# Performance work log

Measured on AMD Instinct MI355X. Metric: run time of the kernel, lower is better.

The kernel has to match this reference:

```python
import jax, jax.numpy as jnp
import numpy as np

B, L, FD = 16, 196, 2048      # batch, fmap locations (14x14), resnet101 feat dim
N, WD, HD, DD = 1000, 300, 512, 5  # n_class, word_dim, hid_dim, d_dim
E, TMAX, NIMG = 50000, 5, 1000     # n_edges, gru steps, imagenet classes


def setup_inputs():
    key = jax.random.key(0)
    ks = jax.random.split(key, 32)
    p = lambda k, s: (jax.random.normal(k, s, jnp.float32) * 0.02)
    z = lambda n: jnp.zeros((n,), jnp.float32)
    return {
        'feats': jax.random.normal(ks[0], (B, L, FD), jnp.float32),
        'embed': jax.random.normal(ks[1], (N, WD), jnp.float32),
        'edges': jax.random.randint(ks[2], (2, E), 0, N, jnp.int32),
        # attention key/query nets
        'W_key': p(ks[3], (FD, HD)), 'b_key': z(HD),
        'W_query': p(ks[4], (WD, HD)), 'b_query': z(HD),
        # F_in: feat_dim -> 512 -> d_dim (relu)
        'Wf1': p(ks[5], (FD, 512)), 'bf1': z(512),
        'Wf2': p(ks[6], (512, DD)), 'bf2': z(DD),
        # F_rel: 2*word_dim -> 256 -> 1 (relu)
        'Wr1': p(ks[7], (2 * WD, 256)), 'br1': z(256),
        'Wr2': p(ks[8], (256, 1)), 'br2': z(1),
        # F_out: d_dim -> 512 -> 1 (relu)
        'Wo1': p(ks[9], (DD, 512)), 'bo1': z(512),
        'Wo2': p(ks[10], (512, 1)), 'bo2': z(1),
        # GRUCell (torch layout: [3*d, d] stacked r,z,n)
        'W_ih': p(ks[11], (3 * DD, DD)), 'b_ih': z(3 * DD),
        'W_hh': p(ks[12], (3 * DD, DD)), 'b_hh': z(3 * DD),
        # imagenet classifier on pooled features
        'W_clf': p(ks[13], (FD, NIMG)), 'b_clf': z(NIMG),
    }


def _gru_cell(x, h, W_ih, W_hh, b_ih, b_hh):
    gi = x @ W_ih.T + b_ih            # [M, 3d]
    gh = h @ W_hh.T + b_hh
    i_r, i_z, i_n = jnp.split(gi, 3, axis=-1)
    h_r, h_z, h_n = jnp.split(gh, 3, axis=-1)
    r = jax.nn.sigmoid(i_r + h_r)
    zg = jax.nn.sigmoid(i_z + h_z)
    n = jnp.tanh(i_n + r * h_n)
    return (1.0 - zg) * n + zg * h


def reference(feats, embed, edges, W_key, b_key, W_query, b_query,
              Wf1, bf1, Wf2, bf2, Wr1, br1, Wr2, br2, Wo1, bo1, Wo2, bo2,
              W_ih, b_ih, W_hh, b_hh, W_clf, b_clf):
    # imagenet scores from globally pooled backbone features
    pooled = jnp.mean(feats, axis=1)                      # [B, FD]
    imgnet_scores = jax.nn.softmax(pooled @ W_clf + b_clf, axis=1)

    # label-conditional spatial attention
    keys = feats @ W_key + b_key                          # [B, L, HD]
    queries = embed @ W_query + b_query                   # [N, HD]
    scores = jnp.einsum('blh,nh->bnl', keys, queries)     # [B, N, L]
    attn = jax.nn.softmax(scores, axis=2)
    graph_input = jnp.einsum('bnl,blf->bnf', attn, feats) # [B, N, FD]
    graph_input = graph_input.reshape(-1, FD)             # [B*N, FD]

    # F_in MLP -> initial hidden state
    h0 = jax.nn.relu(graph_input @ Wf1 + bf1) @ Wf2 + bf2  # [B*N, DD]

    # edge weights from word-embedding pairs, scattered into dense [N, N]
    et = jnp.concatenate([embed[edges[0]], embed[edges[1]]], axis=1)  # [E, 2*WD]
    vals = jnp.tanh((jax.nn.relu(et @ Wr1 + br1) @ Wr2 + br2).reshape(-1))
    prop_mat = jnp.zeros((N, N), jnp.float32).at[edges[0], edges[1]].add(vals)

    # t_max message-passing + GRU steps (sequential recurrence)
    def step(hidden, _):
        msg = jnp.tanh(jnp.einsum('nm,bmd->bnd', prop_mat,
                                  hidden.reshape(B, N, DD))).reshape(-1, DD)
        return _gru_cell(msg, hidden, W_ih, W_hh, b_ih, b_hh), None
    hidden, _ = jax.lax.scan(step, h0, None, length=TMAX)

    logits = (jax.nn.relu(hidden @ Wo1 + bo1) @ Wo2 + bo2).reshape(B, N)
    return logits, attn, imgnet_scores
```

## Files before the change

### kernel.cpp

```cpp
#include <hip/hip_runtime.h>
#include <hip/hip_bf16.h>
#include <math.h>

#define B_   16
#define L_   196
#define FD_  2048
#define N_   1000
#define WD_  300
#define HD_  512
#define DD_  5
#define E_   50000
#define TMAX_ 5
#define NIMG_ 1000
#define WDP_ 320
#define LP_  224
#define EKP_ 640

typedef __attribute__((ext_vector_type(8))) short bf16x8;
typedef __attribute__((ext_vector_type(4))) float f32x4;

#define SMEM_MEGA1    49152
#define SMEM_MM_SPLIT 49152
#define SMEM_MM_NS    24576
#define SMEM_PREP     4352

#define SBAR()    asm volatile("s_barrier" ::: "memory")
#define WVM(N)    asm volatile("s_waitcnt vmcnt(" #N ")" ::: "memory")

__device__ __forceinline__ short bf_hi(float x) {
    unsigned u = __float_as_uint(x);
    unsigned r = u + 0x7fffu + ((u >> 16) & 1u);
    return (short)(r >> 16);
}
__device__ __forceinline__ float bf2f_(short s) {
    return __uint_as_float(((unsigned)(unsigned short)s) << 16);
}

__device__ __forceinline__ void gl16(const short* g, char* l) {
    __builtin_amdgcn_global_load_lds(
        (const __attribute__((address_space(1))) void*)g,
        (__attribute__((address_space(3))) void*)l, 16, 0, 0);
}

#define OUT_SPLIT 1
#define OUT_SC    2
#define OUT_F1T   3
#define OUT_H0    4

template<int OUTMODE, bool SPLIT>
__device__ __forceinline__ void mm_core(
    char* sm, int bx, int by, int zb,
    const short* __restrict__ Ah, const short* __restrict__ Al,
    const short* __restrict__ Bh, const short* __restrict__ Bl,
    const float* __restrict__ bias, void* __restrict__ C0, void* __restrict__ C1,
    void* __restrict__ C2, const float* __restrict__ W2,
    int M, int N, int K, int kbeg, int kend)
{
    const int PBUF = SPLIT ? 24576 : 12288;
    char* AsH = sm;
    char* AsL = sm + 8192;
    char* BsH = sm + (SPLIT ? 16384 : 8192);
    char* BsL = sm + 20480;
    int t = threadIdx.x;
    int lane = t & 63, w = t >> 6;
    int q = lane >> 4, r = lane & 15;
    int row0 = by * 128, col0 = bx * 64;

    int srow = t >> 2, cd = t & 3;
    int cg = cd ^ ((srow >> 1) & 3);
    int gA0 = row0 + srow;       if (gA0 >= M) gA0 = M - 1;
    int gA1 = row0 + 64 + srow;  if (gA1 >= M) gA1 = M - 1;
    int gB  = col0 + srow;       if (gB  >= N) gB  = N - 1;
    const short* pA0 = Ah + (long)gA0 * K + cg * 8 + kbeg;
    const short* pA1 = Ah + (long)gA1 * K + cg * 8 + kbeg;
    const short* pB  = Bh + (long)gB  * K + cg * 8 + kbeg;
    const short* pA0l = Ah; const short* pA1l = Ah; const short* pBl = Bh;
    if (SPLIT) {
        pA0l = Al + (long)gA0 * K + cg * 8 + kbeg;
        pA1l = Al + (long)gA1 * K + cg * 8 + kbeg;
        pBl  = Bl + (long)gB  * K + cg * 8 + kbeg;
    }
    char* dA0 = AsH + t * 16;
    char* dA1 = AsH + 4096 + t * 16;
    char* dB  = BsH + t * 16;
    char* dA0l = AsL + t * 16;
    char* dA1l = AsL + 4096 + t * 16;
    char* dBl  = BsL + t * 16;

    int x = (q ^ ((r >> 1) & 3)) * 16;
    int aoff0 = (w * 32 + r) * 64 + x;
    int aoff1 = aoff0 + 1024;
    int boff[4];
    #pragma unroll
    for (int ct = 0; ct < 4; ct++) boff[ct] = (ct * 16 + r) * 64 + x;

    f32x4 zero4 = {0.f, 0.f, 0.f, 0.f};
    f32x4 acc[2][4];
    #pragma unroll
    for (int i = 0; i < 2; i++)
        #pragma unroll
        for (int j = 0; j < 4; j++) acc[i][j] = zero4;

    auto stage = [&](int ks) {
        int off = (ks & 1) * PBUF;
        int ko = ks * 32;
        gl16(pA0 + ko, dA0 + off);
        gl16(pA1 + ko, dA1 + off);
        gl16(pB  + ko, dB  + off);
        if (SPLIT) {
            gl16(pA0l + ko, dA0l + off);
            gl16(pA1l + ko, dA1l + off);
            gl16(pBl  + ko, dBl  + off);
        }
    };

    int nk = (kend - kbeg) >> 5;
    stage(0);
    for (int ks = 0; ks < nk; ks++) {
        if (ks + 1 < nk) {
            stage(ks + 1);
            if (SPLIT) { WVM(6); } else { WVM(3); }
        } else {
            WVM(0);
        }
        SBAR();

        int cur = (ks & 1) * PBUF;
        bf16x8 ah0 = *(const bf16x8*)(AsH + cur + aoff0);
        bf16x8 ah1 = *(const bf16x8*)(AsH + cur + aoff1);
        bf16x8 al0, al1;
        if (SPLIT) {
            al0 = *(const bf16x8*)(AsL + cur + aoff0);
            al1 = *(const bf16x8*)(AsL + cur + aoff1);
        }
        #pragma unroll
        for (int ct = 0; ct < 4; ct++) {
            bf16x8 bh = *(const bf16x8*)(BsH + cur + boff[ct]);
            acc[0][ct] = __builtin_amdgcn_mfma_f32_16x16x32_bf16(ah0, bh, acc[0][ct], 0, 0, 0);
            acc[1][ct] = __builtin_amdgcn_mfma_f32_16x16x32_bf16(ah1, bh, acc[1][ct], 0, 0, 0);
            if (SPLIT) {
                acc[0][ct] = __builtin_amdgcn_mfma_f32_16x16x32_bf16(al0, bh, acc[0][ct], 0, 0, 0);
                acc[1][ct] = __builtin_amdgcn_mfma_f32_16x16x32_bf16(al1, bh, acc[1][ct], 0, 0, 0);
                bf16x8 bl = *(const bf16x8*)(BsL + cur + boff[ct]);
                acc[0][ct] = __builtin_amdgcn_mfma_f32_16x16x32_bf16(ah0, bl, acc[0][ct], 0, 0, 0);
                acc[1][ct] = __builtin_amdgcn_mfma_f32_16x16x32_bf16(ah1, bl, acc[1][ct], 0, 0, 0);
            }
        }
        if (ks + 1 < nk) SBAR();
    }

    if (OUTMODE == OUT_H0) {
        float s[2][4][DD_];
        #pragma unroll
        for (int i = 0; i < 2; i++)
            #pragma unroll
            for (int reg = 0; reg < 4; reg++)
                #pragma unroll
                for (int d = 0; d < DD_; d++) s[i][reg][d] = 0.f;
        #pragma unroll
        for (int i = 0; i < 2; i++) {
            #pragma unroll
            for (int ct = 0; ct < 4; ct++) {
                int n = col0 + ct * 16 + r;
                float w2v[DD_];
                #pragma unroll
                for (int d = 0; d < DD_; d++) w2v[d] = W2[n * DD_ + d];
                float b1 = bias[n];
                #pragma unroll
                for (int reg = 0; reg < 4; reg++) {
                    int m = row0 + w * 32 + i * 16 + q * 4 + reg;
                    if (m >= M) continue;
                    float val = fmaxf(acc[i][ct][reg] + b1, 0.f);
                    #pragma unroll
                    for (int d = 0; d < DD_; d++) s[i][reg][d] = fmaf(val, w2v[d], s[i][reg][d]);
                }
            }
        }
        #pragma unroll
        for (int i = 0; i < 2; i++)
            #pragma unroll
            for (int reg = 0; reg < 4; reg++)
                #pragma unroll
                for (int d = 0; d < DD_; d++) {
                    float v = s[i][reg][d];
                    v += __shfl_xor(v, 1);
                    v += __shfl_xor(v, 2);
                    v += __shfl_xor(v, 4);
                    v += __shfl_xor(v, 8);
                    if (r == 0) {
                        int m = row0 + w * 32 + i * 16 + q * 4 + reg;
                        if (m < M)
                            atomicAdd(&((float*)C0)[(long)m * (B_ * DD_) + zb * DD_ + d], v);
                    }
                }
        return;
    }

    #pragma unroll
    for (int i = 0; i < 2; i++) {
        #pragma unroll
        for (int ct = 0; ct < 4; ct++) {
            #pragma unroll
            for (int reg = 0; reg < 4; reg++) {
                int m = row0 + w * 32 + i * 16 + q * 4 + reg;
                int n = col0 + ct * 16 + r;
                if (m >= M || n >= N) continue;
                float v = acc[i][ct][reg];
                if (OUTMODE == OUT_SC) {
                    ((float*)C0)[(long)m * N + n] = v;
                } else if (OUTMODE == OUT_F1T) {
                    int b = m / 196, l = m - b * 196;
                    ((short*)C2)[((long)b * 512 + n) * LP_ + l] = bf_hi(v);
                } else {
                    float v2 = v + bias[n];
                    long idx = (long)m * N + n;
                    short hi = bf_hi(v2);
                    ((short*)C0)[idx] = hi;
                    ((short*)C1)[idx] = bf_hi(v2 - bf2f_(hi));
                }
            }
        }
    }
}

__device__ __forceinline__ void edge_core(
    char* sm, int be,
    const short* __restrict__ embedH, const int* __restrict__ edges,
    const short* __restrict__ Wr1T, const float* __restrict__ br1,
    const float* __restrict__ Wr2, const float* __restrict__ br2,
    float* __restrict__ prop)
{
    const int EPBUF = 20480;
    char* As = sm;
    char* Bs = sm + 4096;
    int* src = (int*)(sm + 40960);
    int* dst = (int*)(sm + 41216);
    float (*part)[5] = (float(*)[5])(sm + 41472);
    int t = threadIdx.x;
    int e0 = be * 64;
    if (t < 64) {
        int e = e0 + t;
        src[t] = (e < E_) ? edges[e] : 0;
        dst[t] = (e < E_) ? edges[E_ + e] : 0;
    }
    __syncthreads();
    int lane = t & 63, w = t >> 6, q = lane >> 4, r = lane & 15;
    f32x4 zero4 = {0.f, 0.f, 0.f, 0.f};
    f32x4 acc[4][4];
    #pragma unroll
    for (int i = 0; i < 4; i++)
        #pragma unroll
        for (int j = 0; j < 4; j++) acc[i][j] = zero4;

    int srow = t >> 2, cd = t & 3;
    int cg = cd ^ ((srow >> 1) & 3);
    const short* baseS = embedH + (long)src[srow] * WDP_ + cg * 8;
    const short* baseD = embedH + (long)dst[srow] * WDP_ + cg * 8;
    const short* pB = Wr1T + (long)srow * EKP_ + cg * 8;
    char* dA = As + t * 16;
    char* dB = Bs + t * 16;

    int x = (q ^ ((r >> 1) & 3)) * 16;
    int aoff[4], boff[4];
    #pragma unroll
    for (int i = 0; i < 4; i++) {
        aoff[i] = (i * 16 + r) * 64 + x;
        boff[i] = (w * 64 + i * 16 + r) * 64 + x;
    }

    auto estage = [&](int ks) {
        int off = (ks & 1) * EPBUF;
        const short* pa = (ks < 10) ? baseS + ks * 32 : baseD + (ks - 10) * 32;
        gl16(pa, dA + off);
        #pragma unroll
        for (int i = 0; i < 4; i++)
            gl16(pB + (long)i * 64 * EKP_ + ks * 32, dB + i * 4096 + off);
    };

    estage(0);
    for (int ks = 0; ks < 20; ks++) {
        if (ks + 1 < 20) {
            estage(ks + 1);
            WVM(5);
        } else {
            WVM(0);
        }
        SBAR();

        int cur = (ks & 1) * EPBUF;
        bf16x8 af[4], bfr[4];
        #pragma unroll
        for (int rt = 0; rt < 4; rt++) af[rt] = *(const bf16x8*)(As + cur + aoff[rt]);
        #pragma unroll
        for (int ct = 0; ct < 4; ct++) bfr[ct] = *(const bf16x8*)(Bs + cur + boff[ct]);
        #pragma unroll
        for (int rt = 0; rt < 4; rt++)
            #pragma unroll
            for (int ct = 0; ct < 4; ct++)
                acc[rt][ct] = __builtin_amdgcn_mfma_f32_16x16x32_bf16(af[rt], bfr[ct], acc[rt][ct], 0, 0, 0);
        if (ks + 1 < 20) SBAR();
    }
    float b1v[4], w2v[4];
    #pragma unroll
    for (int ct = 0; ct < 4; ct++) {
        int u = w * 64 + ct * 16 + r;
        b1v[ct] = br1[u];
        w2v[ct] = Wr2[u];
    }
    #pragma unroll
    for (int rt = 0; rt < 4; rt++) {
        #pragma unroll
        for (int reg = 0; reg < 4; reg++) {
            float s = 0.f;
            #pragma unroll
            for (int ct = 0; ct < 4; ct++)
                s = fmaf(fmaxf(acc[rt][ct][reg] + b1v[ct], 0.f), w2v[ct], s);
            s += __shfl_xor(s, 1);
            s += __shfl_xor(s, 2);
            s += __shfl_xor(s, 4);
            s += __shfl_xor(s, 8);
            if (r == 0) part[rt * 16 + q * 4 + reg][w] = s;
        }
    }
    __syncthreads();
    if (t < 64 && e0 + t < E_) {
        float s = part[t][0] + part[t][1] + part[t][2] + part[t][3];
        atomicAdd(&prop[(long)src[t] * N_ + dst[t]], tanhf(s + br2[0]));
    }
}

__device__ __forceinline__ void transconv_core(
    char* sm, int bx, int by,
    const float* __restrict__ in, short* __restrict__ outH, short* __restrict__ outL,
    int Kd, int N, int Ks)
{
    float (*tile)[33] = (float(*)[33])sm;
    int k0 = bx * 32, n0 = by * 32;
    int t = threadIdx.x;
    int tr = t >> 5, tc = t & 31;
    #pragma unroll
    for (int i = 0; i < 4; i++) {
        int k = k0 + tr + i * 8, n = n0 + tc;
        tile[tr + i * 8][tc] = (k < Kd && n < N) ? in[(long)k * N + n] : 0.f;
    }
    __syncthreads();
    #pragma unroll
    for (int i = 0; i < 4; i++) {
        int n = n0 + tr + i * 8, k = k0 + tc;
        if (n < N && k < Ks) {
            float x = tile[tc][tr + i * 8];
            short hi = bf_hi(x);
            outH[(long)n * Ks + k] = hi;
            if (outL) outL[(long)n * Ks + k] = bf_hi(x - bf2f_(hi));
        }
    }
}

__global__ __launch_bounds__(256) void prep(
    float* __restrict__ prop, float* __restrict__ Ht0, const float* __restrict__ bf2,
    const float* __restrict__ feats, float* __restrict__ pooled,
    short* __restrict__ featsH, short* __restrict__ featsL,
    const float* __restrict__ embed, short* __restrict__ embH, short* __restrict__ embL,
    const float* __restrict__ W_key, const float* __restrict__ Wf1,
    short* __restrict__ WkfH, short* __restrict__ WkfL,
    const float* __restrict__ W_query, short* __restrict__ WqTh, short* __restrict__ WqTl,
    const float* __restrict__ Wr1, short* __restrict__ Wr1T, short* __restrict__ F1T)
{
    __shared__ __align__(16) char sm[SMEM_PREP];
    int b = blockIdx.x, t = threadIdx.x;
    if (b < 977) {
        int i = (b * 256 + t) * 4;
        if (i < N_ * N_) { float4 z = {0.f, 0.f, 0.f, 0.f}; *(float4*)(prop + i) = z; }
    } else if (b < 1290) {
        int i = (b - 977) * 256 + t;
        if (i < N_ * B_ * DD_) Ht0[i] = bf2[i % DD_];
    } else if (b < 1322) {
        int idx = (b - 1290) * 256 + t;
        int bb = idx >> 9, f4 = (idx & 511) * 4;
        const float* p = feats + (long)bb * L_ * FD_ + f4;
        float4 acc = {0.f, 0.f, 0.f, 0.f};
        for (int l = 0; l < L_; l++) {
            float4 v = *(const float4*)(p + (long)l * FD_);
            acc.x += v.x; acc.y += v.y; acc.z += v.z; acc.w += v.w;
        }
        const float inv = 1.0f / L_;
        acc.x *= inv; acc.y *= inv; acc.z *= inv; acc.w *= inv;
        *(float4*)(pooled + (long)bb * FD_ + f4) = acc;
    } else if (b < 4458) {
        long i = ((long)(b - 1322) * 256 + t) * 8;
        float4 v0 = *(const float4*)(feats + i);
        float4 v1 = *(const float4*)(feats + i + 4);
        float xs[8] = {v0.x, v0.y, v0.z, v0.w, v1.x, v1.y, v1.z, v1.w};
        short h[8], l8[8];
        #pragma unroll
        for (int j = 0; j < 8; j++) {
            h[j] = bf_hi(xs[j]);
            l8[j] = bf_hi(xs[j] - bf2f_(h[j]));
        }
        *(int4*)(featsH + i) = *(int4*)h;
        *(int4*)(featsL + i) = *(int4*)l8;
    } else if (b < 4771) {
        int i = ((b - 4458) * 256 + t) * 4;
        if (i < N_ * WDP_) {
            int n = i / WDP_, c = i - n * WDP_;
            short h[4], l4[4];
            if (c < WD_) {
                float4 v = *(const float4*)(embed + (long)n * WD_ + c);
                float xs[4] = {v.x, v.y, v.z, v.w};
                #pragma unroll
                for (int j = 0; j < 4; j++) {
                    h[j] = bf_hi(xs[j]);
                    l4[j] = bf_hi(xs[j] - bf2f_(h[j]));
                }
            } else {
                #pragma unroll
                for (int j = 0; j < 4; j++) { h[j] = 0; l4[j] = 0; }
            }
            *(int2*)(embH + (long)n * WDP_ + c) = *(int2*)h;
            *(int2*)(embL + (long)n * WDP_ + c) = *(int2*)l4;
        }
    } else if (b < 5795) {
        int bb = b - 4771;
        transconv_core(sm, bb % 64, bb / 64, W_key, WkfH, WkfL, FD_, HD_, FD_);
    } else if (b < 6819) {
        int bb = b - 5795;
        transconv_core(sm, bb % 64, bb / 64, Wf1, WkfH + (size_t)512 * FD_, nullptr, FD_, HD_, FD_);
    } else if (b < 6979) {
        int bb = b - 6819;
        transconv_core(sm, bb % 10, bb / 10, W_query, WqTh, WqTl, WD_, HD_, WDP_);
    } else if (b < 7139) {
        int bb = b - 6979;
        int bx = bb % 20, by = bb / 20;
        float (*tile)[33] = (float(*)[33])sm;
        int k0 = bx * 32, n0 = by * 32;
        int tr = t >> 5, tc = t & 31;
        #pragma unroll
        for (int i = 0; i < 4; i++) {
            int kout = k0 + tr + i * 8, n = n0 + tc;
            int kin = (kout < 320) ? kout : kout - 20;
            bool valid = (kout < 320) ? (kout < 300) : (kout < 620);
            tile[tr + i * 8][tc] = valid ? Wr1[(long)kin * 256 + n] : 0.f;
        }
        __syncthreads();
        #pragma unroll
        for (int i = 0; i < 4; i++) {
            int n = n0 + tr + i * 8, k = k0 + tc;
            Wr1T[(long)n * EKP_ + k] = bf_hi(tile[tc][tr + i * 8]);
        }
    } else {
        int idx = (b - 7139) * 256 + t;
        int row = idx / 7, j = idx - row * 7;
        int2 z2; z2.x = 0; z2.y = 0;
        *(int2*)(F1T + (long)row * LP_ + 196 + j * 4) = z2;
    }
}

__global__ __launch_bounds__(256) void mega1(
    const short* __restrict__ featsH, const short* __restrict__ featsL,
    const short* __restrict__ WkfH, const short* __restrict__ WkfL,
    const float* __restrict__ b_key, short* __restrict__ keysH, short* __restrict__ keysL,
    short* __restrict__ F1T,
    const short* __restrict__ embH, const short* __restrict__ embL,
    const short* __restrict__ WqTh, const short* __restrict__ WqTl,
    const float* __restrict__ b_query, short* __restrict__ qH, short* __restrict__ qL,
    const int* __restrict__ edges, const short* __restrict__ Wr1T,
    const float* __restrict__ br1, const float* __restrict__ Wr2,
    const float* __restrict__ br2, float* __restrict__ prop,
    const float* __restrict__ pooled, const float* __restrict__ W_clf,
    const float* __restrict__ b_clf, float* __restrict__ Pimg)
{
    __shared__ __align__(16) char sm[SMEM_MEGA1];
    int b = blockIdx.x;
    if (b < 200) {
        int l = (b & 7) * 25 + (b >> 3);
        mm_core<OUT_SPLIT, true>(sm, l & 7, l >> 3, 0,
            featsH, featsL, WkfH, WkfL, b_key,
            keysH, keysL, nullptr, nullptr, B_ * L_, 512, FD_, 0, FD_);
    } else if (b < 400) {
        int bb = b - 200;
        int l = (bb & 7) * 25 + (bb >> 3);
        mm_core<OUT_F1T, false>(sm, l & 7, l >> 3, 0,
            featsH, nullptr, WkfH + (size_t)512 * FD_, nullptr, nullptr,
            nullptr, nullptr, F1T, nullptr, B_ * L_, 512, FD_, 0, FD_);
    } else if (b < 464) {
        int bb = b - 400;
        int l = (bb & 7) * 8 + (bb >> 3);
        mm_core<OUT_SPLIT, true>(sm, l & 7, l >> 3, 0,
            embH, embL, WqTh, WqTl, b_query,
            qH, qL, nullptr, nullptr, N_, HD_, WDP_, 0, WDP_);
    } else if (b < 1246) {
        edge_core(sm, b - 464, embH, edges, Wr1T, br1, Wr2, br2, prop);
    } else {
        int bb = b - 1246;
        int ks = bb / 63, ix = bb % 63;
        int i = ix * 256 + threadIdx.x;
        if (i < B_ * NIMG_) {
            int bi = i / NIMG_, n = i % NIMG_;
            const float* p = pooled + (long)bi * FD_ + ks * 256;
            const float* w = W_clf + (long)(ks * 256) * NIMG_ + n;
            float acc = (ks == 0) ? b_clf[n] : 0.f;
            #pragma unroll 4
            for (int k = 0; k < 256; k++) acc = fmaf(p[k], w[(long)k * NIMG_], acc);
            Pimg[(long)ks * (B_ * NIMG_) + i] = acc;
        }
    }
}

__global__ __launch_bounds__(256) void mega2(
    const short* __restrict__ qH, const short* __restrict__ qL,
    const short* __restrict__ keysH, const short* __restrict__ keysL,
    float* __restrict__ Pattn,
    const float* __restrict__ Pimg, float* __restrict__ out_img)
{
    __shared__ __align__(16) char sm[SMEM_MM_SPLIT];
    int b = blockIdx.x;
    if (b < 512) {
        int l = (b & 7) * 64 + (b >> 3);
        int zb = l >> 5, by = (l >> 2) & 7, bx = l & 3;
        const short* Bh = keysH + (long)zb * L_ * HD_;
        const short* Bl = keysL + (long)zb * L_ * HD_;
        float* C0 = Pattn + (long)zb * N_ * L_;
        mm_core<OUT_SC, true>(sm, bx, by, 0, qH, qL, Bh, Bl, nullptr,
                              C0, nullptr, nullptr, nullptr,
                              N_, L_, HD_, 0, HD_);
    } else {
        int t = threadIdx.x;
        int wave = (b - 512) * 4 + (t >> 6), lane = t & 63;
        if (wave >= B_) return;
        const int PER = (NIMG_ + 63) / 64;
        float v[PER];
        float m = -1e30f;
        int cnt = 0;
        for (int k = lane; k < NIMG_; k += 64) {
            float s = 0.f;
            #pragma unroll
            for (int ks = 0; ks < 8; ks++) s += Pimg[(long)ks * (B_ * NIMG_) + wave * NIMG_ + k];
            v[cnt] = s; m = fmaxf(m, s); cnt++;
        }
        #pragma unroll
        for (int off = 32; off; off >>= 1) m = fmaxf(m, __shfl_xor(m, off));
        float s = 0.f;
        for (int i = 0; i < cnt; i++) { v[i] = expf(v[i] - m); s += v[i]; }
        #pragma unroll
        for (int off = 32; off; off >>= 1) s += __shfl_xor(s, off);
        float inv = 1.f / s;
        cnt = 0;
        for (int k = lane; k < NIMG_; k += 64) out_img[(long)wave * NIMG_ + k] = v[cnt++] * inv;
    }
}

__global__ void softmax_attn(const float* __restrict__ P0,
                             float* __restrict__ X, short* __restrict__ Xb, int rows)
{
    int gid = blockIdx.x * blockDim.x + threadIdx.x;
    int wave = gid >> 6, lane = gid & 63;
    if (wave >= rows) return;
    const int PER = (L_ + 63) / 64;
    float v[PER];
    float m = -1e30f;
    int cnt = 0;
    for (int k = lane; k < L_; k += 64) {
        v[cnt] = P0[(long)wave * L_ + k];
        m = fmaxf(m, v[cnt]); cnt++;
    }
    #pragma unroll
    for (int off = 32; off; off >>= 1) m = fmaxf(m, __shfl_xor(m, off));
    float s = 0.f;
    for (int i = 0; i < cnt; i++) { v[i] = expf(v[i] - m); s += v[i]; }
    #pragma unroll
    for (int off = 32; off; off >>= 1) s += __shfl_xor(s, off);
    float inv = 1.f / s;
    cnt = 0;
    for (int k = lane; k < L_; k += 64) {
        float val = v[cnt++] * inv;
        X[(long)wave * L_ + k] = val;
        Xb[(long)wave * LP_ + k] = bf_hi(val);
    }
    if (lane < LP_ - L_) Xb[(long)wave * LP_ + L_ + lane] = 0;
}

__global__ __launch_bounds__(256) void h0gemm(
    const short* __restrict__ attnH, const short* __restrict__ F1T,
    const float* __restrict__ bf1, const float* __restrict__ Wf2,
    float* __restrict__ Ht0)
{
    __shared__ __align__(16) char sm[SMEM_MM_NS];
    int b = blockIdx.x;
    int l = (b & 7) * 128 + (b >> 3);
    int zb = l >> 6, by = (l >> 3) & 7, bx = l & 7;
    const short* Ap = attnH + (long)zb * N_ * LP_;
    const short* Bp = F1T + (long)zb * HD_ * LP_;
    mm_core<OUT_H0, false>(sm, bx, by, zb, Ap, nullptr, Bp, nullptr,
                           bf1, Ht0, nullptr, nullptr, Wf2,
                           N_, HD_, LP_, 0, LP_);
}

__global__ __launch_bounds__(640) void step_kernel(
    const float* __restrict__ prop, const float* __restrict__ Hin,
    float* __restrict__ Hout,
    const float* __restrict__ W_ih, const float* __restrict__ b_ih,
    const float* __restrict__ W_hh, const float* __restrict__ b_hh)
{
    __shared__ float msg[2][4][80];
    int t = threadIdx.x;
    int half = t / 320, tt = t - half * 320;
    int nl = tt / 80, c = tt - nl * 80;
    int n = blockIdx.x * 4 + nl;
    const float* pr = prop + (long)n * N_ + half * 500;
    const float* hc = Hin + c + (long)half * 500 * 80;
    float a0 = 0.f, a1 = 0.f, a2 = 0.f, a3 = 0.f;
    #pragma unroll 4
    for (int m4 = 0; m4 < 500; m4 += 4) {
        float4 pv = *(const float4*)(pr + m4);
        a0 = fmaf(pv.x, hc[(long)(m4 + 0) * 80], a0);
        a1 = fmaf(pv.y, hc[(long)(m4 + 1) * 80], a1);
        a2 = fmaf(pv.z, hc[(long)(m4 + 2) * 80], a2);
        a3 = fmaf(pv.w, hc[(long)(m4 + 3) * 80], a3);
    }
    msg[half][nl][c] = (a0 + a1) + (a2 + a3);
    __syncthreads();
    if (t < 320) {
        int nl2 = t / 80, c2 = t - nl2 * 80;
        msg[0][nl2][c2] = tanhf(msg[0][nl2][c2] + msg[1][nl2][c2]);
    }
    __syncthreads();
    if (t < 64) {
        int nl2 = t >> 4, b = t & 15;
        int n2 = blockIdx.x * 4 + nl2;
        float xv[DD_], h[DD_];
        #pragma unroll
        for (int j = 0; j < DD_; j++) {
            xv[j] = msg[0][nl2][b * DD_ + j];
            h[j] = Hin[(long)n2 * 80 + b * DD_ + j];
        }
        float gi[3 * DD_], gh[3 * DD_];
        #pragma unroll
        for (int g = 0; g < 3 * DD_; g++) {
            float a = b_ih[g], cc = b_hh[g];
            #pragma unroll
            for (int k = 0; k < DD_; k++) {
                a = fmaf(xv[k], W_ih[g * DD_ + k], a);
                cc = fmaf(h[k], W_hh[g * DD_ + k], cc);
            }
            gi[g] = a; gh[g] = cc;
        }
        #pragma unroll
        for (int j = 0; j < DD_; j++) {
            float rr = 1.f / (1.f + expf(-(gi[j] + gh[j])));
            float zz = 1.f / (1.f + expf(-(gi[DD_ + j] + gh[DD_ + j])));
            float nn2 = tanhf(gi[2 * DD_ + j] + rr * gh[2 * DD_ + j]);
            Hout[(long)n2 * 80 + b * DD_ + j] = (1.f - zz) * nn2 + zz * h[j];
        }
    }
}

__global__ __launch_bounds__(256) void out_kernel(
    const float* __restrict__ ht, const float* __restrict__ Wo1,
    const float* __restrict__ bo1, const float* __restrict__ Wo2,
    const float* __restrict__ bo2, float* __restrict__ logits, int rows)
{
    __shared__ float w1[DD_][HD_];
    __shared__ float w2[HD_];
    __shared__ float b1[HD_];
    int t = threadIdx.x;
    for (int j = t; j < HD_; j += 256) {
        w2[j] = Wo2[j];
        b1[j] = bo1[j];
        #pragma unroll
        for (int d = 0; d < DD_; d++) w1[d][j] = Wo1[d * HD_ + j];
    }
    __syncthreads();
    int wv = t >> 6, lane = t & 63;
    float bo2v = bo2[0];
    #pragma unroll
    for (int rr = 0; rr < 16; rr++) {
        int row = blockIdx.x * 64 + wv * 16 + rr;
        if (row >= rows) break;
        int b = row / N_, n = row - b * N_;
        float x[DD_];
        #pragma unroll
        for (int i = 0; i < DD_; i++) x[i] = ht[(long)n * (B_ * DD_) + b * DD_ + i];
        float acc = 0.f;
        for (int j = lane; j < HD_; j += 64) {
            float h = b1[j];
            #pragma unroll
            for (int d = 0; d < DD_; d++) h = fmaf(x[d], w1[d][j], h);
            h = fmaxf(h, 0.f);
            acc = fmaf(h, w2[j], acc);
        }
        #pragma unroll
        for (int off = 32; off; off >>= 1) acc += __shfl_down(acc, off);
        if (lane == 0) logits[row] = acc + bo2v;
    }
}

extern "C" void kernel_launch(void* const* d_in, const int* in_sizes, int n_in,
                              void* d_out, int out_size, void* d_ws, size_t ws_size,
                              hipStream_t stream)
{
    const float* feats   = (const float*)d_in[0];
    const float* embed   = (const float*)d_in[1];
    const int*   edges   = (const int*)  d_in[2];
    const float* W_key   = (const float*)d_in[3];
    const float* b_key   = (const float*)d_in[4];
    const float* W_query = (const float*)d_in[5];
    const float* b_query = (const float*)d_in[6];
    const float* Wf1     = (const float*)d_in[7];
    const float* bf1     = (const float*)d_in[8];
    const float* Wf2     = (const float*)d_in[9];
    const float* bf2     = (const float*)d_in[10];
    const float* Wr1     = (const float*)d_in[11];
    const float* br1     = (const float*)d_in[12];
    const float* Wr2     = (const float*)d_in[13];
    const float* br2     = (const float*)d_in[14];
    const float* Wo1     = (const float*)d_in[15];
    const float* bo1     = (const float*)d_in[16];
    const float* Wo2     = (const float*)d_in[17];
    const float* bo2     = (const float*)d_in[18];
    const float* W_ih    = (const float*)d_in[19];
    const float* b_ih    = (const float*)d_in[20];
    const float* W_hh    = (const float*)d_in[21];
    const float* b_hh    = (const float*)d_in[22];
    const float* W_clf   = (const float*)d_in[23];
    const float* b_clf   = (const float*)d_in[24];

    float* out_logits = (float*)d_out;
    float* out_attn   = out_logits + B_ * N_;
    float* out_img    = out_attn + (long)B_ * N_ * L_;

    char* p = (char*)d_ws;
    auto alloc = [&](size_t bytes) { void* r = (void*)p; p += (bytes + 255) & ~(size_t)255; return r; };
    float* pooled  = (float*)alloc((size_t)B_ * FD_ * 4);
    short* featsH  = (short*)alloc((size_t)B_ * L_ * FD_ * 2);
    short* featsL  = (short*)alloc((size_t)B_ * L_ * FD_ * 2);
    short* WkfH    = (short*)alloc((size_t)1024 * FD_ * 2);
    short* WkfL    = (short*)alloc((size_t)512 * FD_ * 2);
    short* WqTh    = (short*)alloc((size_t)HD_ * WDP_ * 2);
    short* WqTl    = (short*)alloc((size_t)HD_ * WDP_ * 2);
    short* Wr1T    = (short*)alloc((size_t)256 * EKP_ * 2);
    short* embH    = (short*)alloc((size_t)N_ * WDP_ * 2);
    short* embL    = (short*)alloc((size_t)N_ * WDP_ * 2);
    short* keysH   = (short*)alloc((size_t)B_ * L_ * HD_ * 2);
    short* keysL   = (short*)alloc((size_t)B_ * L_ * HD_ * 2);
    short* qH      = (short*)alloc((size_t)N_ * HD_ * 2);
    short* qL      = (short*)alloc((size_t)N_ * HD_ * 2);
    short* attnH   = (short*)alloc((size_t)B_ * N_ * LP_ * 2);
    short* F1T     = (short*)alloc((size_t)B_ * HD_ * LP_ * 2);
    float* prop    = (float*)alloc((size_t)N_ * N_ * 4);
    float* Ht0     = (float*)alloc((size_t)N_ * B_ * DD_ * 4);
    float* Ht1     = (float*)alloc((size_t)N_ * B_ * DD_ * 4);
    float* Pimg    = (float*)alloc((size_t)8 * B_ * NIMG_ * 4);
    float* Pattn   = (float*)alloc((size_t)B_ * N_ * L_ * 4);

    prep<<<7363, 256, 0, stream>>>(prop, Ht0, bf2, feats, pooled, featsH, featsL,
                                   embed, embH, embL, W_key, Wf1, WkfH, WkfL,
                                   W_query, WqTh, WqTl, Wr1, Wr1T, F1T);

    mega1<<<1750, 256, 0, stream>>>(featsH, featsL, WkfH, WkfL, b_key, keysH, keysL, F1T,
                                    embH, embL, WqTh, WqTl, b_query, qH, qL,
                                    edges, Wr1T, br1, Wr2, br2, prop,
                                    pooled, W_clf, b_clf, Pimg);

    mega2<<<516, 256, 0, stream>>>(qH, qL, keysH, keysL, Pattn, Pimg, out_img);

    softmax_attn<<<(B_ * N_ * 64 + 255) / 256, 256, 0, stream>>>(
        Pattn, out_attn, attnH, B_ * N_);

    h0gemm<<<1024, 256, 0, stream>>>(attnH, F1T, bf1, Wf2, Ht0);

    {
        float* hin = Ht0;
        float* hout = Ht1;
        for (int step = 0; step < TMAX_; step++) {
            step_kernel<<<N_ / 4, 640, 0, stream>>>(prop, hin, hout,
                                                    W_ih, b_ih, W_hh, b_hh);
            float* tmp = hin; hin = hout; hout = tmp;
        }
        out_kernel<<<250, 256, 0, stream>>>(hin, Wo1, bo1, Wo2, bo2,
                                            out_logits, B_ * N_);
    }
}
```

Baseline: 448.9 us.

## Fuse GRU recurrence steps and output MLP into one persistent kernel with grid barrier

Replaces the five step_kernel launches plus out_kernel with a single persistent kernel of 250 blocks. The blocks synchronise between steps through an atomic counter barrier in global memory, and prep resets that counter. The aim is to remove per-launch overhead and idle gaps between the small sequential kernels. It relies on all 250 blocks of 640 threads being co-resident, since otherwise the barrier spins forever. It also depends on __threadfence for visibility of hidden-state writes across blocks.

```diff
diff --git a/kernel.cpp b/kernel.cpp
--- a/kernel.cpp
+++ b/kernel.cpp
@@ -364,7 +364,8 @@
     const float* __restrict__ W_key, const float* __restrict__ Wf1,
     short* __restrict__ WkfH, short* __restrict__ WkfL,
     const float* __restrict__ W_query, short* __restrict__ WqTh, short* __restrict__ WqTl,
-    const float* __restrict__ Wr1, short* __restrict__ Wr1T, short* __restrict__ F1T)
+    const float* __restrict__ Wr1, short* __restrict__ Wr1T, short* __restrict__ F1T,
+    unsigned* __restrict__ bar)
 {
     __shared__ __align__(16) char sm[SMEM_PREP];
     int b = blockIdx.x, t = threadIdx.x;
@@ -447,11 +448,13 @@
             int n = n0 + tr + i * 8, k = k0 + tc;
             Wr1T[(long)n * EKP_ + k] = bf_hi(tile[tc][tr + i * 8]);
         }
-    } else {
+    } else if (b < 7363) {
         int idx = (b - 7139) * 256 + t;
         int row = idx / 7, j = idx - row * 7;
         int2 z2; z2.x = 0; z2.y = 0;
         *(int2*)(F1T + (long)row * LP_ + 196 + j * 4) = z2;
+    } else {
+        if (t < 8) bar[t] = 0;
     }
 }
 
@@ -595,91 +598,100 @@
                            N_, HD_, LP_, 0, LP_);
 }
 
-__global__ __launch_bounds__(640) void step_kernel(
-    const float* __restrict__ prop, const float* __restrict__ Hin,
-    float* __restrict__ Hout,
+__global__ __launch_bounds__(640) void recur_out(
+    const float* __restrict__ prop, float* __restrict__ Ht0, float* __restrict__ Ht1,
     const float* __restrict__ W_ih, const float* __restrict__ b_ih,
-    const float* __restrict__ W_hh, const float* __restrict__ b_hh)
+    const float* __restrict__ W_hh, const float* __restrict__ b_hh,
+    const float* __restrict__ Wo1, const float* __restrict__ bo1,
+    const float* __restrict__ Wo2, const float* __restrict__ bo2,
+    float* __restrict__ logits, unsigned* __restrict__ bar)
 {
     __shared__ float msg[2][4][80];
-    int t = threadIdx.x;
-    int half = t / 320, tt = t - half * 320;
-    int nl = tt / 80, c = tt - nl * 80;
-    int n = blockIdx.x * 4 + nl;
-    const float* pr = prop + (long)n * N_ + half * 500;
-    const float* hc = Hin + c + (long)half * 500 * 80;
-    float a0 = 0.f, a1 = 0.f, a2 = 0.f, a3 = 0.f;
-    #pragma unroll 4
-    for (int m4 = 0; m4 < 500; m4 += 4) {
-        float4 pv = *(const float4*)(pr + m4);
-        a0 = fmaf(pv.x, hc[(long)(m4 + 0) * 80], a0);
-        a1 = fmaf(pv.y, hc[(long)(m4 + 1) * 80], a1);
-        a2 = fmaf(pv.z, hc[(long)(m4 + 2) * 80], a2);
-        a3 = fmaf(pv.w, hc[(long)(m4 + 3) * 80], a3);
-    }
-    msg[half][nl][c] = (a0 + a1) + (a2 + a3);
-    __syncthreads();
-    if (t < 320) {
-        int nl2 = t / 80, c2 = t - nl2 * 80;
-        msg[0][nl2][c2] = tanhf(msg[0][nl2][c2] + msg[1][nl2][c2]);
-    }
-    __syncthreads();
-    if (t < 64) {
-        int nl2 = t >> 4, b = t & 15;
-        int n2 = blockIdx.x * 4 + nl2;
-        float xv[DD_], h[DD_];
-        #pragma unroll
-        for (int j = 0; j < DD_; j++) {
-            xv[j] = msg[0][nl2][b * DD_ + j];
-            h[j] = Hin[(long)n2 * 80 + b * DD_ + j];
-        }
-        float gi[3 * DD_], gh[3 * DD_];
-        #pragma unroll
-        for (int g = 0; g < 3 * DD_; g++) {
-            float a = b_ih[g], cc = b_hh[g];
-            #pragma unroll
-            for (int k = 0; k < DD_; k++) {
-                a = fmaf(xv[k], W_ih[g * DD_ + k], a);
-                cc = fmaf(h[k], W_hh[g * DD_ + k], cc);
-            }
-            gi[g] = a; gh[g] = cc;
-        }
-        #pragma unroll
-        for (int j = 0; j < DD_; j++) {
-            float rr = 1.f / (1.f + expf(-(gi[j] + gh[j])));
-            float zz = 1.f / (1.f + expf(-(gi[DD_ + j] + gh[DD_ + j])));
-            float nn2 = tanhf(gi[2 * DD_ + j] + rr * gh[2 * DD_ + j]);
-            Hout[(long)n2 * 80 + b * DD_ + j] = (1.f - zz) * nn2 + zz * h[j];
-        }
-    }
-}
-
-__global__ __launch_bounds__(256) void out_kernel(
-    const float* __restrict__ ht, const float* __restrict__ Wo1,
-    const float* __restrict__ bo1, const float* __restrict__ Wo2,
-    const float* __restrict__ bo2, float* __restrict__ logits, int rows)
-{
     __shared__ float w1[DD_][HD_];
     __shared__ float w2[HD_];
     __shared__ float b1[HD_];
     int t = threadIdx.x;
-    for (int j = t; j < HD_; j += 256) {
+    for (int j = t; j < HD_; j += 640) {
         w2[j] = Wo2[j];
         b1[j] = bo1[j];
         #pragma unroll
         for (int d = 0; d < DD_; d++) w1[d][j] = Wo1[d * HD_ + j];
     }
-    __syncthreads();
+
+    float* hin = Ht0;
+    float* hout = Ht1;
+    int half = t / 320, tt = t - half * 320;
+    int nl = tt / 80, c = tt - nl * 80;
+    int n = blockIdx.x * 4 + nl;
+
+    for (int step = 0; step < TMAX_; step++) {
+        const float* pr = prop + (long)n * N_ + half * 500;
+        const float* hc = hin + c + (long)half * 500 * 80;
+        float a0 = 0.f, a1 = 0.f, a2 = 0.f, a3 = 0.f;
+        #pragma unroll 4
+        for (int m4 = 0; m4 < 500; m4 += 4) {
+            float4 pv = *(const float4*)(pr + m4);
+            a0 = fmaf(pv.x, hc[(long)(m4 + 0) * 80], a0);
+            a1 = fmaf(pv.y, hc[(long)(m4 + 1) * 80], a1);
+            a2 = fmaf(pv.z, hc[(long)(m4 + 2) * 80], a2);
+            a3 = fmaf(pv.w, hc[(long)(m4 + 3) * 80], a3);
+        }
+        msg[half][nl][c] = (a0 + a1) + (a2 + a3);
+        __syncthreads();
+        if (t < 320) {
+            int nl2 = t / 80, c2 = t - nl2 * 80;
+            msg[0][nl2][c2] = tanhf(msg[0][nl2][c2] + msg[1][nl2][c2]);
+        }
+        __syncthreads();
+        if (t < 64) {
+            int nl2 = t >> 4, bb = t & 15;
+            int n2 = blockIdx.x * 4 + nl2;
+            float xv[DD_], h[DD_];
+            #pragma unroll
+            for (int j = 0; j < DD_; j++) {
+                xv[j] = msg[0][nl2][bb * DD_ + j];
+                h[j] = hin[(long)n2 * 80 + bb * DD_ + j];
+            }
+            float gi[3 * DD_], gh[3 * DD_];
+            #pragma unroll
+            for (int g = 0; g < 3 * DD_; g++) {
+                float a = b_ih[g], cc = b_hh[g];
+                #pragma unroll
+                for (int k = 0; k < DD_; k++) {
+                    a = fmaf(xv[k], W_ih[g * DD_ + k], a);
+                    cc = fmaf(h[k], W_hh[g * DD_ + k], cc);
+                }
+                gi[g] = a; gh[g] = cc;
+            }
+            #pragma unroll
+            for (int j = 0; j < DD_; j++) {
+                float rr = 1.f / (1.f + expf(-(gi[j] + gh[j])));
+                float zz = 1.f / (1.f + expf(-(gi[DD_ + j] + gh[DD_ + j])));
+                float nn2 = tanhf(gi[2 * DD_ + j] + rr * gh[2 * DD_ + j]);
+                hout[(long)n2 * 80 + bb * DD_ + j] = (1.f - zz) * nn2 + zz * h[j];
+            }
+        }
+        { float* tmp = hin; hin = hout; hout = tmp; }
+
+        __threadfence();
+        __syncthreads();
+        if (t == 0) {
+            atomicAdd(&bar[step], 1u);
+            while (atomicAdd(&bar[step], 0u) < (unsigned)(N_ / 4))
+                __builtin_amdgcn_s_sleep(2);
+        }
+        __syncthreads();
+        __threadfence();
+    }
+
     int wv = t >> 6, lane = t & 63;
     float bo2v = bo2[0];
-    #pragma unroll
-    for (int rr = 0; rr < 16; rr++) {
-        int row = blockIdx.x * 64 + wv * 16 + rr;
-        if (row >= rows) break;
-        int b = row / N_, n = row - b * N_;
+    for (int ri = wv; ri < 64; ri += 10) {
+        int row = blockIdx.x * 64 + ri;
+        int b = row / N_, nn = row - b * N_;
         float x[DD_];
         #pragma unroll
-        for (int i = 0; i < DD_; i++) x[i] = ht[(long)n * (B_ * DD_) + b * DD_ + i];
+        for (int i = 0; i < DD_; i++) x[i] = hin[(long)nn * (B_ * DD_) + b * DD_ + i];
         float acc = 0.f;
         for (int j = lane; j < HD_; j += 64) {
             float h = b1[j];
@@ -751,10 +763,11 @@
     float* Ht1     = (float*)alloc((size_t)N_ * B_ * DD_ * 4);
     float* Pimg    = (float*)alloc((size_t)8 * B_ * NIMG_ * 4);
     float* Pattn   = (float*)alloc((size_t)B_ * N_ * L_ * 4);
-
-    prep<<<7363, 256, 0, stream>>>(prop, Ht0, bf2, feats, pooled, featsH, featsL,
+    unsigned* bar  = (unsigned*)alloc(256);
+
+    prep<<<7364, 256, 0, stream>>>(prop, Ht0, bf2, feats, pooled, featsH, featsL,
                                    embed, embH, embL, W_key, Wf1, WkfH, WkfL,
-                                   W_query, WqTh, WqTl, Wr1, Wr1T, F1T);
+                                   W_query, WqTh, WqTl, Wr1, Wr1T, F1T, bar);
 
     mega1<<<1750, 256, 0, stream>>>(featsH, featsL, WkfH, WkfL, b_key, keysH, keysL, F1T,
                                     embH, embL, WqTh, WqTl, b_query, qH, qL,
@@ -768,15 +781,6 @@
 
     h0gemm<<<1024, 256, 0, stream>>>(attnH, F1T, bf1, Wf2, Ht0);
 
-    {
-        float* hin = Ht0;
-        float* hout = Ht1;
-        for (int step = 0; step < TMAX_; step++) {
-            step_kernel<<<N_ / 4, 640, 0, stream>>>(prop, hin, hout,
-                                                    W_ih, b_ih, W_hh, b_hh);
-            float* tmp = hin; hin = hout; hout = tmp;
-        }
-        out_kernel<<<250, 256, 0, stream>>>(hin, Wo1, bo1, Wo2, bo2,
-                                            out_logits, B_ * N_);
-    }
-}
+    recur_out<<<250, 640, 0, stream>>>(prop, Ht0, Ht1, W_ih, b_ih, W_hh, b_hh,
+                                       Wo1, bo1, Wo2, bo2, out_logits, bar);
+}
```

Measured after the change: 882.1 us. 96.5% more time.

## Reuse hidden-state loads across four output rows in GRU step kernel

Applied to the files above, without the earlier changes.

Restructures the message-passing step so each thread computes four output rows over a quarter of the m range, reusing each loaded hidden value across four prop rows instead of one. Thread count per block drops from 640 to 320, and partial sums are reduced through shared memory across four m-segments. This cuts redundant global loads of the hidden state. The cost is fewer threads in flight and narrower float2 prop loads, which may lower memory-level parallelism.

```diff
diff --git a/kernel.cpp b/kernel.cpp
--- a/kernel.cpp
+++ b/kernel.cpp
@@ -595,54 +595,61 @@
                            N_, HD_, LP_, 0, LP_);
 }
 
-__global__ __launch_bounds__(640) void step_kernel(
+__global__ __launch_bounds__(320) void step_kernel(
     const float* __restrict__ prop, const float* __restrict__ Hin,
     float* __restrict__ Hout,
     const float* __restrict__ W_ih, const float* __restrict__ b_ih,
     const float* __restrict__ W_hh, const float* __restrict__ b_hh)
 {
-    __shared__ float msg[2][4][80];
+    __shared__ float part[4][4][80];
+    __shared__ float msg[4][80];
     int t = threadIdx.x;
-    int half = t / 320, tt = t - half * 320;
-    int nl = tt / 80, c = tt - nl * 80;
-    int n = blockIdx.x * 4 + nl;
-    const float* pr = prop + (long)n * N_ + half * 500;
-    const float* hc = Hin + c + (long)half * 500 * 80;
+    int g = t / 80, c = t - g * 80;
+    int n0 = blockIdx.x * 4;
+    int m0 = g * 250;
+    const float* hc = Hin + (long)m0 * 80 + c;
+    const float* pr = prop + (long)n0 * N_ + m0;
     float a0 = 0.f, a1 = 0.f, a2 = 0.f, a3 = 0.f;
-    #pragma unroll 4
-    for (int m4 = 0; m4 < 500; m4 += 4) {
-        float4 pv = *(const float4*)(pr + m4);
-        a0 = fmaf(pv.x, hc[(long)(m4 + 0) * 80], a0);
-        a1 = fmaf(pv.y, hc[(long)(m4 + 1) * 80], a1);
-        a2 = fmaf(pv.z, hc[(long)(m4 + 2) * 80], a2);
-        a3 = fmaf(pv.w, hc[(long)(m4 + 3) * 80], a3);
-    }
-    msg[half][nl][c] = (a0 + a1) + (a2 + a3);
+    #pragma unroll 2
+    for (int m2 = 0; m2 < 250; m2 += 2) {
+        float h0 = hc[(long)(m2 + 0) * 80];
+        float h1 = hc[(long)(m2 + 1) * 80];
+        float2 p0 = *(const float2*)(pr + 0 * N_ + m2);
+        float2 p1 = *(const float2*)(pr + 1 * N_ + m2);
+        float2 p2 = *(const float2*)(pr + 2 * N_ + m2);
+        float2 p3 = *(const float2*)(pr + 3 * N_ + m2);
+        a0 = fmaf(p0.x, h0, a0); a0 = fmaf(p0.y, h1, a0);
+        a1 = fmaf(p1.x, h0, a1); a1 = fmaf(p1.y, h1, a1);
+        a2 = fmaf(p2.x, h0, a2); a2 = fmaf(p2.y, h1, a2);
+        a3 = fmaf(p3.x, h0, a3); a3 = fmaf(p3.y, h1, a3);
+    }
+    part[g][0][c] = a0;
+    part[g][1][c] = a1;
+    part[g][2][c] = a2;
+    part[g][3][c] = a3;
     __syncthreads();
-    if (t < 320) {
-        int nl2 = t / 80, c2 = t - nl2 * 80;
-        msg[0][nl2][c2] = tanhf(msg[0][nl2][c2] + msg[1][nl2][c2]);
-    }
+    msg[g][c] = tanhf((part[0][g][c] + part[1][g][c]) +
+                      (part[2][g][c] + part[3][g][c]));
     __syncthreads();
     if (t < 64) {
         int nl2 = t >> 4, b = t & 15;
-        int n2 = blockIdx.x * 4 + nl2;
+        int n2 = n0 + nl2;
         float xv[DD_], h[DD_];
         #pragma unroll
         for (int j = 0; j < DD_; j++) {
-            xv[j] = msg[0][nl2][b * DD_ + j];
+            xv[j] = msg[nl2][b * DD_ + j];
             h[j] = Hin[(long)n2 * 80 + b * DD_ + j];
         }
         float gi[3 * DD_], gh[3 * DD_];
         #pragma unroll
-        for (int g = 0; g < 3 * DD_; g++) {
-            float a = b_ih[g], cc = b_hh[g];
+        for (int gg = 0; gg < 3 * DD_; gg++) {
+            float a = b_ih[gg], cc = b_hh[gg];
             #pragma unroll
             for (int k = 0; k < DD_; k++) {
-                a = fmaf(xv[k], W_ih[g * DD_ + k], a);
-                cc = fmaf(h[k], W_hh[g * DD_ + k], cc);
+                a = fmaf(xv[k], W_ih[gg * DD_ + k], a);
+                cc = fmaf(h[k], W_hh[gg * DD_ + k], cc);
             }
-            gi[g] = a; gh[g] = cc;
+            gi[gg] = a; gh[gg] = cc;
         }
         #pragma unroll
         for (int j = 0; j < DD_; j++) {
@@ -772,7 +779,7 @@
         float* hin = Ht0;
         float* hout = Ht1;
         for (int step = 0; step < TMAX_; step++) {
-            step_kernel<<<N_ / 4, 640, 0, stream>>>(prop, hin, hout,
+            step_kernel<<<N_ / 4, 320, 0, stream>>>(prop, hin, hout,
                                                     W_ih, b_ih, W_hh, b_hh);
             float* tmp = hin; hin = hout; hout = tmp;
         }
```

Result: slower. 538.6 us (+20.0%).
